# Performance work log

Hardware: AMD Instinct MI355X
Metric: run time of the kernel (lower is better)

Reference implementation:

```python
import jax, jax.numpy as jnp
import numpy as np

EPS = 1e-5
QMAX = 127.0   # 8-bit symmetric: representable range [-128, 127]
QMIN = -128.0


def ste_round(x):
    # straight-through rounding (identity gradient)
    return x + jax.lax.stop_gradient(jnp.round(x) - x)


def setup_inputs() -> dict:
    key = jax.random.key(0)
    ks = jax.random.split(key, 7)
    N, C_in, C_out, H, W = 64, 256, 128, 56, 56
    x = jax.random.normal(ks[0], (N, C_in, H, W), jnp.float32)
    act_scaling_factor = jax.random.uniform(ks[1], (1,), jnp.float32, 0.02, 0.08)
    bn_weight = 1.0 + 0.3 * jax.random.normal(ks[2], (C_in,), jnp.float32)
    bn_bias = 0.1 * jax.random.normal(ks[3], (C_in,), jnp.float32)
    bn_mean = 0.1 * jax.random.normal(ks[4], (C_in,), jnp.float32)
    bn_var = jax.random.uniform(ks[5], (C_in,), jnp.float32, 0.5, 1.5)
    conv_weight = 0.05 * jax.random.normal(ks[6], (C_out, C_in, 1, 1), jnp.float32)
    return {
        "x": x,
        "act_scaling_factor": act_scaling_factor,
        "bn_weight": bn_weight,
        "bn_bias": bn_bias,
        "bn_mean": bn_mean,
        "bn_var": bn_var,
        "conv_weight": conv_weight,
    }


def _fwd(x, act_scaling_factor, bn_weight, bn_bias, bn_mean, bn_var, conv_weight):
    act_sf = act_scaling_factor.reshape(())

    # ---- QuantBn: fold BN, quantize folded scale per-channel (8-bit symmetric) ----
    inv_std = jax.lax.rsqrt(bn_var + EPS)
    scale = bn_weight * inv_std                    # [C_in]
    shift = bn_bias - bn_mean * scale              # [C_in]
    bn_sf = jnp.max(jnp.abs(scale)) / QMAX         # per-tensor bn weight scale
    scale_q = jnp.clip(ste_round(scale / bn_sf), QMIN, QMAX) * bn_sf
    bias_sf = bn_sf * act_sf                        # bias quantized at combined scale
    shift_q = ste_round(shift / bias_sf) * bias_sf
    x = x * scale_q[None, :, None, None] + shift_q[None, :, None, None]

    # ---- ReLU ----
    x = jnp.maximum(x, 0.0)

    # ---- QuantAct 1: per-tensor symmetric 8-bit requant ----
    sf1 = jnp.max(jnp.abs(x)) / QMAX
    x = jnp.clip(ste_round(x / sf1), QMIN, QMAX) * sf1

    # ---- QuantConv2d: per-output-channel 8-bit symmetric weight quant, 1x1 conv ----
    w_sf = jnp.max(jnp.abs(conv_weight), axis=(1, 2, 3)) / QMAX   # [C_out]
    w_q = jnp.clip(ste_round(conv_weight / w_sf[:, None, None, None]), QMIN, QMAX) \
          * w_sf[:, None, None, None]
    y = jax.lax.conv_general_dilated(
        x, w_q, window_strides=(1, 1), padding='VALID',
        dimension_numbers=('NCHW', 'OIHW', 'NCHW'))

    # ---- QuantAct 2 ----
    sf2 = jnp.max(jnp.abs(y)) / QMAX
    y = jnp.clip(ste_round(y / sf2), QMIN, QMAX) * sf2

    # ---- QuantAveragePool2d (2x2, stride 2): average in integer domain, re-round ----
    N, C, H, W = y.shape
    y_int = (y / sf2).reshape(N, C, H // 2, 2, W // 2, 2).mean(axis=(3, 5))
    out = ste_round(y_int) * sf2
    return out, sf2


def reference(x, act_scaling_factor, bn_weight, bn_bias, bn_mean, bn_var, conv_weight):
    return _fwd(x, act_scaling_factor, bn_weight, bn_bias, bn_mean, bn_var, conv_weight)
```

## Files before the change

### kernel.cpp

```cpp
#include <hip/hip_runtime.h>

#define QMAXF 127.0f
typedef int i32x4 __attribute__((ext_vector_type(4)));

__device__ __forceinline__ unsigned fkey(float f) {
  const unsigned b = __float_as_uint(f);
  return (b & 0x80000000u) ? ~b : (b | 0x80000000u);
}
__device__ __forceinline__ float fdec(unsigned u) {
  return __uint_as_float((u & 0x80000000u) ? (u & 0x7FFFFFFFu) : ~u);
}

__global__ __launch_bounds__(256) void k0_zero(unsigned* __restrict__ p) {
  const int t = threadIdx.x;
  p[t] = 0u; p[t + 256] = 0u; p[t + 512] = 0u; p[t + 768] = 0u;
}

__global__ __launch_bounds__(256, 8) void k1_minmax(
    const float* __restrict__ x, const float* __restrict__ actsf,
    const float* __restrict__ bnw, const float* __restrict__ bnb,
    const float* __restrict__ bnm, const float* __restrict__ bnv,
    const float* __restrict__ cw, unsigned* __restrict__ chanKmx,
    unsigned* __restrict__ chanKmn, float* __restrict__ scq,
    float* __restrict__ shq, float* __restrict__ wsf,
    signed char* __restrict__ wq8) {
  const int t = threadIdx.x, b = blockIdx.x;
  if (b == 2048) {
    __shared__ float red[4];
    float scale, shift;
    {
#pragma clang fp contract(off)
      float inv = 1.0f / sqrtf(bnv[t] + 1e-5f);
      scale = bnw[t] * inv;
      float tmp = bnm[t] * scale;
      shift = bnb[t] - tmp;
    }
    float a = fabsf(scale);
    for (int o = 32; o > 0; o >>= 1) a = fmaxf(a, __shfl_xor(a, o));
    if ((t & 63) == 0) red[t >> 6] = a;
    __syncthreads();
    const float amax = fmaxf(fmaxf(red[0], red[1]), fmaxf(red[2], red[3]));
    const float bn_sf = amax / QMAXF;
    scq[t] = fminf(fmaxf(rintf(scale / bn_sf), -128.f), 127.f) * bn_sf;
    const float bias_sf = bn_sf * actsf[0];
    shq[t] = rintf(shift / bias_sf) * bias_sf;
    const int r = t >> 1, half = t & 1;
    const float4* wrow = (const float4*)(cw + r * 256 + half * 128);
    float mx = 0.f;
#pragma unroll
    for (int j = 0; j < 32; ++j) {
      const float4 v = wrow[j];
      mx = fmaxf(mx, fmaxf(fmaxf(fabsf(v.x), fabsf(v.y)), fmaxf(fabsf(v.z), fabsf(v.w))));
    }
    mx = fmaxf(mx, __shfl_xor(mx, 1));
    const float wsf_v = mx / QMAXF;
    if (half == 0) wsf[r] = wsf_v;
    int* w8w = (int*)wq8;
#pragma unroll
    for (int j = 0; j < 32; ++j) {
      const float4 v = wrow[j];
      const float q0 = fminf(fmaxf(rintf(v.x / wsf_v), -128.f), 127.f);
      const float q1 = fminf(fmaxf(rintf(v.y / wsf_v), -128.f), 127.f);
      const float q2 = fminf(fmaxf(rintf(v.z / wsf_v), -128.f), 127.f);
      const float q3 = fminf(fmaxf(rintf(v.w / wsf_v), -128.f), 127.f);
      w8w[r * 64 + half * 32 + j] =
          ((int)q0 & 255) | (((int)q1 & 255) << 8) | (((int)q2 & 255) << 16) | (((int)q3 & 255) << 24);
    }
    return;
  }
  __shared__ float redmn[4][8], redmx[4][8];
  const int n = b >> 5, cg = b & 31;
  const float4* __restrict__ x4 = (const float4*)x + (long)(n * 256 + cg * 8) * 784;
  float mn[8], mx[8];
#pragma unroll
  for (int r = 0; r < 8; ++r) { mn[r] = __builtin_inff(); mx[r] = -__builtin_inff(); }
#pragma unroll
  for (int r = 0; r < 8; ++r) {
    const float4* row = x4 + r * 784;
    for (int j = t; j < 784; j += 256) {
      const float4 v = row[j];
      mn[r] = fminf(mn[r], fminf(fminf(v.x, v.y), fminf(v.z, v.w)));
      mx[r] = fmaxf(mx[r], fmaxf(fmaxf(v.x, v.y), fmaxf(v.z, v.w)));
    }
  }
#pragma unroll
  for (int r = 0; r < 8; ++r)
    for (int o = 32; o > 0; o >>= 1) {
      mn[r] = fminf(mn[r], __shfl_xor(mn[r], o));
      mx[r] = fmaxf(mx[r], __shfl_xor(mx[r], o));
    }
  if ((t & 63) == 0) {
#pragma unroll
    for (int r = 0; r < 8; ++r) { redmn[t >> 6][r] = mn[r]; redmx[t >> 6][r] = mx[r]; }
  }
  __syncthreads();
  if (t < 8) {
    const float fmn = fminf(fminf(redmn[0][t], redmn[1][t]), fminf(redmn[2][t], redmn[3][t]));
    const float fmx = fmaxf(fmaxf(redmx[0][t], redmx[1][t]), fmaxf(redmx[2][t], redmx[3][t]));
    atomicMax(&chanKmx[cg * 8 + t], fkey(fmx));
    atomicMax(&chanKmn[cg * 8 + t], ~fkey(fmn));
  }
}

__global__ __launch_bounds__(256, 4) void k2f_quant_gemm(
    const float* __restrict__ x, const float* __restrict__ scq,
    const float* __restrict__ shq, const unsigned* __restrict__ chanKmx,
    const unsigned* __restrict__ chanKmn, const signed char* __restrict__ wq8,
    const float* __restrict__ wsf, signed char* __restrict__ xqT,
    float* __restrict__ blockmax) {
  __shared__ int sw[64 * 64];
  __shared__ float comax[128];
  __shared__ float red[4];
  __shared__ float sf1s;
  const int t = threadIdx.x, w = t >> 6, l = t & 63, m = l & 15, g = l >> 4;
  const int blk = blockIdx.x, n = blk / 49, tt = blk - n * 49;

  {
    const float s = scq[t], sh = shq[t];
    const float xe = (s >= 0.f) ? fdec(chanKmx[t]) : fdec(~chanKmn[t]);
    float z;
    {
#pragma clang fp contract(off)
      z = xe * s + sh;
    }
    float mm = fmaxf(z, 0.f);
    for (int o = 32; o > 0; o >>= 1) mm = fmaxf(mm, __shfl_xor(mm, o));
    if (l == 0) red[w] = mm;
    __syncthreads();
    if (t == 0) sf1s = fmaxf(fmaxf(red[0], red[1]), fmaxf(red[2], red[3])) / QMAXF;
    __syncthreads();
  }
  const float sf1 = sf1s;
  const float* __restrict__ xb = x + (long)n * 802816 + tt * 64;

  signed char* __restrict__ dst = xqT + ((long)(n * 3136 + tt * 64)) * 256;
  {
    const int slot = t & 15, hwq = t >> 4;
    const int hw0 = hwq * 4, ci0 = slot * 16;
    int wbuf[4][4] = {{0, 0, 0, 0}, {0, 0, 0, 0}, {0, 0, 0, 0}, {0, 0, 0, 0}};
#pragma unroll
    for (int j = 0; j < 16; ++j) {
      const float4 v = *(const float4*)(xb + (long)(ci0 + j) * 3136 + hw0);
      const float s = scq[ci0 + j], sh = shq[ci0 + j];
      float z0, z1, z2, z3;
      {
#pragma clang fp contract(off)
        z0 = v.x * s + sh; z1 = v.y * s + sh; z2 = v.z * s + sh; z3 = v.w * s + sh;
      }
      const float q0 = fminf(fmaxf(rintf(fmaxf(z0, 0.f) / sf1), -128.f), 127.f);
      const float q1 = fminf(fmaxf(rintf(fmaxf(z1, 0.f) / sf1), -128.f), 127.f);
      const float q2 = fminf(fmaxf(rintf(fmaxf(z2, 0.f) / sf1), -128.f), 127.f);
      const float q3 = fminf(fmaxf(rintf(fmaxf(z3, 0.f) / sf1), -128.f), 127.f);
      wbuf[0][j >> 2] |= ((int)q0 & 255) << ((j & 3) * 8);
      wbuf[1][j >> 2] |= ((int)q1 & 255) << ((j & 3) * 8);
      wbuf[2][j >> 2] |= ((int)q2 & 255) << ((j & 3) * 8);
      wbuf[3][j >> 2] |= ((int)q3 & 255) << ((j & 3) * 8);
    }
#pragma unroll
    for (int dh = 0; dh < 4; ++dh) {
      const int hw = hw0 + dh;
      *(i32x4*)&sw[hw * 64 + ((slot ^ (hw & 7)) << 2)] = *(const i32x4*)wbuf[dh];
      *(i32x4*)(dst + hw * 256 + slot * 16) = *(const i32x4*)wbuf[dh];
    }
  }
  __syncthreads();

  i32x4 acc[2][4];
#pragma unroll
  for (int ct = 0; ct < 2; ++ct)
#pragma unroll
    for (int ht = 0; ht < 4; ++ht) acc[ct][ht] = (i32x4){0, 0, 0, 0};
#pragma unroll
  for (int ks = 0; ks < 4; ++ks) {
    const i32x4 wf0 = *(const i32x4*)(wq8 + (w * 32 + m) * 256 + ks * 64 + g * 16);
    const i32x4 wf1 = *(const i32x4*)(wq8 + (w * 32 + 16 + m) * 256 + ks * 64 + g * 16);
#pragma unroll
    for (int ht = 0; ht < 4; ++ht) {
      const int row = ht * 16 + m;
      const i32x4 xf = *(const i32x4*)&sw[row * 64 + (((ks * 4 + g) ^ (row & 7)) << 2)];
      acc[0][ht] = __builtin_amdgcn_mfma_i32_16x16x64_i8(wf0, xf, acc[0][ht], 0, 0, 0);
      acc[1][ht] = __builtin_amdgcn_mfma_i32_16x16x64_i8(wf1, xf, acc[1][ht], 0, 0, 0);
    }
  }

  int im[2][4];
#pragma unroll
  for (int ct = 0; ct < 2; ++ct)
#pragma unroll
    for (int r = 0; r < 4; ++r) {
      int v = 0;
#pragma unroll
      for (int ht = 0; ht < 4; ++ht) {
        int a = acc[ct][ht][r];
        a = a < 0 ? -a : a;
        v = a > v ? a : v;
      }
      im[ct][r] = v;
    }
#pragma unroll
  for (int o = 1; o < 16; o <<= 1)
#pragma unroll
    for (int ct = 0; ct < 2; ++ct)
#pragma unroll
      for (int r = 0; r < 4; ++r) {
        const int other = __shfl_xor(im[ct][r], o);
        im[ct][r] = other > im[ct][r] ? other : im[ct][r];
      }
  if (m == 0) {
#pragma unroll
    for (int ct = 0; ct < 2; ++ct)
#pragma unroll
      for (int r = 0; r < 4; ++r)
        comax[w * 32 + ct * 16 + g * 4 + r] = (float)im[ct][r];
  }
  __syncthreads();
  float v = 0.f;
  if (t < 128) v = comax[t] * (sf1 * wsf[t]);
  for (int o = 32; o > 0; o >>= 1) v = fmaxf(v, __shfl_xor(v, o));
  if (l == 0) red[w] = v;
  __syncthreads();
  if (t == 0)
    blockmax[blk] = fmaxf(fmaxf(red[0], red[1]), fmaxf(red[2], red[3]));
}

__global__ __launch_bounds__(256, 3) void k3_final(
    const signed char* __restrict__ xqT, const signed char* __restrict__ wq8,
    const float* __restrict__ wsf, const float* __restrict__ scq,
    const float* __restrict__ shq, const unsigned* __restrict__ chanKmx,
    const unsigned* __restrict__ chanKmn, const float* __restrict__ blockmax,
    float* __restrict__ out, float* __restrict__ outsf2) {
  __shared__ _Float16 q2[128 * 116];
  __shared__ float red[4];
  __shared__ float sf1s, sf2s;
  const int t = threadIdx.x, w = t >> 6, l = t & 63;
  const int m = l & 15, g = l >> 4;
  const int blk = blockIdx.x;
  const int n = blk / 28, tt = blk - n * 28;

  {
    const float s = scq[t], sh = shq[t];
    const float xe = (s >= 0.f) ? fdec(chanKmx[t]) : fdec(~chanKmn[t]);
    float z;
    {
#pragma clang fp contract(off)
      z = xe * s + sh;
    }
    float mm = fmaxf(z, 0.f);
    for (int o = 32; o > 0; o >>= 1) mm = fmaxf(mm, __shfl_xor(mm, o));
    if (l == 0) red[w] = mm;
    __syncthreads();
    if (t == 0) sf1s = fmaxf(fmaxf(red[0], red[1]), fmaxf(red[2], red[3])) / QMAXF;
  }
  {
    float bm = 0.f;
    for (int i = t; i < 3136; i += 256) bm = fmaxf(bm, blockmax[i]);
    for (int o = 32; o > 0; o >>= 1) bm = fmaxf(bm, __shfl_xor(bm, o));
    __syncthreads();
    if (l == 0) red[w] = bm;
    __syncthreads();
    if (t == 0) sf2s = fmaxf(fmaxf(red[0], red[1]), fmaxf(red[2], red[3])) / QMAXF;
    __syncthreads();
  }
  const float sf1 = sf1s;
  const float sf2 = sf2s;
  if (blk == 0 && t == 0) outsf2[0] = sf2;

  const signed char* __restrict__ xb = xqT + ((long)(n * 3136 + tt * 112)) * 256;
  i32x4 acc[2][7];
#pragma unroll
  for (int ct = 0; ct < 2; ++ct)
#pragma unroll
    for (int ht = 0; ht < 7; ++ht) acc[ct][ht] = (i32x4){0, 0, 0, 0};
#pragma unroll
  for (int ks = 0; ks < 4; ++ks) {
    const i32x4 wf0 = *(const i32x4*)(wq8 + (w * 32 + m) * 256 + ks * 64 + g * 16);
    const i32x4 wf1 = *(const i32x4*)(wq8 + (w * 32 + 16 + m) * 256 + ks * 64 + g * 16);
#pragma unroll
    for (int ht = 0; ht < 7; ++ht) {
      const i32x4 xf = *(const i32x4*)(xb + (ht * 16 + m) * 256 + ks * 64 + g * 16);
      acc[0][ht] = __builtin_amdgcn_mfma_i32_16x16x64_i8(wf0, xf, acc[0][ht], 0, 0, 0);
      acc[1][ht] = __builtin_amdgcn_mfma_i32_16x16x64_i8(wf1, xf, acc[1][ht], 0, 0, 0);
    }
  }
  float fac[2][4];
#pragma unroll
  for (int ct = 0; ct < 2; ++ct)
#pragma unroll
    for (int r = 0; r < 4; ++r)
      fac[ct][r] = sf1 * wsf[w * 32 + ct * 16 + g * 4 + r];
#pragma unroll
  for (int ct = 0; ct < 2; ++ct)
#pragma unroll
    for (int ht = 0; ht < 7; ++ht)
#pragma unroll
      for (int r = 0; r < 4; ++r) {
        const float y = (float)acc[ct][ht][r] * fac[ct][r];
        const float q = fminf(fmaxf(rintf(y / sf2), -128.f), 127.f);
        q2[(w * 32 + ct * 16 + g * 4 + r) * 116 + ht * 16 + m] = (_Float16)q;
      }
  __syncthreads();
  const long obase = (long)n * 100352 + tt * 28;
  for (int i = t; i < 3584; i += 256) {
    const unsigned co = (unsigned)i / 28u;
    const unsigned wo = (unsigned)i - co * 28u;
    const _Float16* row = q2 + co * 116;
    const float a = (float)row[2 * wo] + (float)row[2 * wo + 1] +
                    (float)row[56 + 2 * wo] + (float)row[56 + 2 * wo + 1];
    out[obase + (long)co * 784 + wo] = rintf(a * 0.25f) * sf2;
  }
}

extern "C" void kernel_launch(void* const* d_in, const int* in_sizes, int n_in,
                              void* d_out, int out_size, void* d_ws, size_t ws_size,
                              hipStream_t stream) {
  const float* x     = (const float*)d_in[0];
  const float* actsf = (const float*)d_in[1];
  const float* bnw   = (const float*)d_in[2];
  const float* bnb   = (const float*)d_in[3];
  const float* bnm   = (const float*)d_in[4];
  const float* bnv   = (const float*)d_in[5];
  const float* cw    = (const float*)d_in[6];
  float* out = (float*)d_out;
  char* ws = (char*)d_ws;

  unsigned* chanKmx   = (unsigned*)(ws + 256);
  unsigned* chanKmn   = (unsigned*)(ws + 1280);
  float* scq          = (float*)(ws + 4096);
  float* shq          = (float*)(ws + 5120);
  float* wsf          = (float*)(ws + 6144);
  signed char* wq8    = (signed char*)(ws + 8192);
  float* blockmax     = (float*)(ws + 40960);
  signed char* xqT    = (signed char*)(ws + 65536);
  float* outsf2       = out + (out_size - 1);

  hipLaunchKernelGGL(k0_zero, dim3(1), dim3(256), 0, stream, (unsigned*)ws);
  hipLaunchKernelGGL(k1_minmax, dim3(2049), dim3(256), 0, stream,
                     x, actsf, bnw, bnb, bnm, bnv, cw, chanKmx, chanKmn, scq, shq, wsf, wq8);
  hipLaunchKernelGGL(k2f_quant_gemm, dim3(3136), dim3(256), 0, stream,
                     x, scq, shq, chanKmx, chanKmn, wq8, wsf, xqT, blockmax);
  hipLaunchKernelGGL(k3_final, dim3(1792), dim3(256), 0, stream,
                     xqT, wq8, wsf, scq, shq, chanKmx, chanKmn, blockmax, out, outsf2);
}
```

Baseline: 157.1 us.

## Enlarge quant-GEMM tile to 112 pixels with byte-granular swizzled LDS transpose

The fused quantize+GEMM kernel now processes 112 spatial positions per block instead of 64, cutting the grid from 3136 to 1792 blocks and the blockmax array accordingly. Loads are remapped so consecutive threads read contiguous float4 along HW, and quantized bytes are scattered into an XOR-swizzled LDS tile that is then read back as 16-byte rows both for the global xqT write and for the MFMA operands. BN scale/shift are cached in shared memory. The aim is better coalescing of x reads and fewer blocks, at the cost of byte-wide LDS stores, more LDS per block and more accumulator registers.

```diff
diff --git a/kernel.cpp b/kernel.cpp
--- a/kernel.cpp
+++ b/kernel.cpp
@@ -108,15 +108,17 @@
     const unsigned* __restrict__ chanKmn, const signed char* __restrict__ wq8,
     const float* __restrict__ wsf, signed char* __restrict__ xqT,
     float* __restrict__ blockmax) {
-  __shared__ int sw[64 * 64];
+  __shared__ __align__(16) unsigned char ldsb[112 * 256];
+  __shared__ float s_scq[256], s_shq[256];
   __shared__ float comax[128];
   __shared__ float red[4];
   __shared__ float sf1s;
   const int t = threadIdx.x, w = t >> 6, l = t & 63, m = l & 15, g = l >> 4;
-  const int blk = blockIdx.x, n = blk / 49, tt = blk - n * 49;
+  const int blk = blockIdx.x, n = blk / 28, tt = blk - n * 28;
 
   {
     const float s = scq[t], sh = shq[t];
+    s_scq[t] = s; s_shq[t] = sh;
     const float xe = (s >= 0.f) ? fdec(chanKmx[t]) : fdec(~chanKmn[t]);
     float z;
     {
@@ -131,53 +133,55 @@
     __syncthreads();
   }
   const float sf1 = sf1s;
-  const float* __restrict__ xb = x + (long)n * 802816 + tt * 64;
-
-  signed char* __restrict__ dst = xqT + ((long)(n * 3136 + tt * 64)) * 256;
-  {
-    const int slot = t & 15, hwq = t >> 4;
-    const int hw0 = hwq * 4, ci0 = slot * 16;
-    int wbuf[4][4] = {{0, 0, 0, 0}, {0, 0, 0, 0}, {0, 0, 0, 0}, {0, 0, 0, 0}};
-#pragma unroll
-    for (int j = 0; j < 16; ++j) {
-      const float4 v = *(const float4*)(xb + (long)(ci0 + j) * 3136 + hw0);
-      const float s = scq[ci0 + j], sh = shq[ci0 + j];
-      float z0, z1, z2, z3;
-      {
+  const float* __restrict__ xb = x + (long)n * 802816 + tt * 112;
+
+  for (int it = 0; it < 28; ++it) {
+    const int idx = it * 256 + t;
+    const int c = idx / 28;
+    const int p = idx - c * 28;
+    const float4 v = *(const float4*)(xb + (long)c * 3136 + 4 * p);
+    const float s = s_scq[c], sh = s_shq[c];
+    float z0, z1, z2, z3;
+    {
 #pragma clang fp contract(off)
-        z0 = v.x * s + sh; z1 = v.y * s + sh; z2 = v.z * s + sh; z3 = v.w * s + sh;
-      }
-      const float q0 = fminf(fmaxf(rintf(fmaxf(z0, 0.f) / sf1), -128.f), 127.f);
-      const float q1 = fminf(fmaxf(rintf(fmaxf(z1, 0.f) / sf1), -128.f), 127.f);
-      const float q2 = fminf(fmaxf(rintf(fmaxf(z2, 0.f) / sf1), -128.f), 127.f);
-      const float q3 = fminf(fmaxf(rintf(fmaxf(z3, 0.f) / sf1), -128.f), 127.f);
-      wbuf[0][j >> 2] |= ((int)q0 & 255) << ((j & 3) * 8);
-      wbuf[1][j >> 2] |= ((int)q1 & 255) << ((j & 3) * 8);
-      wbuf[2][j >> 2] |= ((int)q2 & 255) << ((j & 3) * 8);
-      wbuf[3][j >> 2] |= ((int)q3 & 255) << ((j & 3) * 8);
-    }
-#pragma unroll
-    for (int dh = 0; dh < 4; ++dh) {
-      const int hw = hw0 + dh;
-      *(i32x4*)&sw[hw * 64 + ((slot ^ (hw & 7)) << 2)] = *(const i32x4*)wbuf[dh];
-      *(i32x4*)(dst + hw * 256 + slot * 16) = *(const i32x4*)wbuf[dh];
-    }
-  }
-  __syncthreads();
-
-  i32x4 acc[2][4];
-#pragma unroll
-  for (int ct = 0; ct < 2; ++ct)
-#pragma unroll
-    for (int ht = 0; ht < 4; ++ht) acc[ct][ht] = (i32x4){0, 0, 0, 0};
+      z0 = v.x * s + sh; z1 = v.y * s + sh; z2 = v.z * s + sh; z3 = v.w * s + sh;
+    }
+    const float q0 = fminf(fmaxf(rintf(fmaxf(z0, 0.f) / sf1), -128.f), 127.f);
+    const float q1 = fminf(fmaxf(rintf(fmaxf(z1, 0.f) / sf1), -128.f), 127.f);
+    const float q2 = fminf(fmaxf(rintf(fmaxf(z2, 0.f) / sf1), -128.f), 127.f);
+    const float q3 = fminf(fmaxf(rintf(fmaxf(z3, 0.f) / sf1), -128.f), 127.f);
+    const int cs = c ^ ((p & 15) << 4);
+    const int hw0 = 4 * p;
+    ldsb[(hw0 + 0) * 256 + cs] = (unsigned char)((int)q0 & 255);
+    ldsb[(hw0 + 1) * 256 + cs] = (unsigned char)((int)q1 & 255);
+    ldsb[(hw0 + 2) * 256 + cs] = (unsigned char)((int)q2 & 255);
+    ldsb[(hw0 + 3) * 256 + cs] = (unsigned char)((int)q3 & 255);
+  }
+  __syncthreads();
+
+  signed char* __restrict__ dst = xqT + ((long)(n * 3136 + tt * 112)) * 256;
+#pragma unroll
+  for (int it = 0; it < 7; ++it) {
+    const int idx = it * 256 + t;
+    const int hw = idx >> 4, c16 = idx & 15;
+    const i32x4 v = *(const i32x4*)&ldsb[hw * 256 + ((c16 * 16) ^ (((hw >> 2) & 15) << 4))];
+    *(i32x4*)(dst + hw * 256 + c16 * 16) = v;
+  }
+
+  i32x4 acc[2][7];
+#pragma unroll
+  for (int ct = 0; ct < 2; ++ct)
+#pragma unroll
+    for (int ht = 0; ht < 7; ++ht) acc[ct][ht] = (i32x4){0, 0, 0, 0};
 #pragma unroll
   for (int ks = 0; ks < 4; ++ks) {
     const i32x4 wf0 = *(const i32x4*)(wq8 + (w * 32 + m) * 256 + ks * 64 + g * 16);
     const i32x4 wf1 = *(const i32x4*)(wq8 + (w * 32 + 16 + m) * 256 + ks * 64 + g * 16);
 #pragma unroll
-    for (int ht = 0; ht < 4; ++ht) {
+    for (int ht = 0; ht < 7; ++ht) {
       const int row = ht * 16 + m;
-      const i32x4 xf = *(const i32x4*)&sw[row * 64 + (((ks * 4 + g) ^ (row & 7)) << 2)];
+      const i32x4 xf = *(const i32x4*)&ldsb[row * 256 +
+                          ((ks * 64 + g * 16) ^ (((row >> 2) & 15) << 4))];
       acc[0][ht] = __builtin_amdgcn_mfma_i32_16x16x64_i8(wf0, xf, acc[0][ht], 0, 0, 0);
       acc[1][ht] = __builtin_amdgcn_mfma_i32_16x16x64_i8(wf1, xf, acc[1][ht], 0, 0, 0);
     }
@@ -190,7 +194,7 @@
     for (int r = 0; r < 4; ++r) {
       int v = 0;
 #pragma unroll
-      for (int ht = 0; ht < 4; ++ht) {
+      for (int ht = 0; ht < 7; ++ht) {
         int a = acc[ct][ht][r];
         a = a < 0 ? -a : a;
         v = a > v ? a : v;
@@ -253,7 +257,7 @@
   }
   {
     float bm = 0.f;
-    for (int i = t; i < 3136; i += 256) bm = fmaxf(bm, blockmax[i]);
+    for (int i = t; i < 1792; i += 256) bm = fmaxf(bm, blockmax[i]);
     for (int o = 32; o > 0; o >>= 1) bm = fmaxf(bm, __shfl_xor(bm, o));
     __syncthreads();
     if (l == 0) red[w] = bm;
@@ -336,7 +340,7 @@
   hipLaunchKernelGGL(k0_zero, dim3(1), dim3(256), 0, stream, (unsigned*)ws);
   hipLaunchKernelGGL(k1_minmax, dim3(2049), dim3(256), 0, stream,
                      x, actsf, bnw, bnb, bnm, bnv, cw, chanKmx, chanKmn, scq, shq, wsf, wq8);
-  hipLaunchKernelGGL(k2f_quant_gemm, dim3(3136), dim3(256), 0, stream,
+  hipLaunchKernelGGL(k2f_quant_gemm, dim3(1792), dim3(256), 0, stream,
                      x, scq, shq, chanKmx, chanKmn, wq8, wsf, xqT, blockmax);
   hipLaunchKernelGGL(k3_final, dim3(1792), dim3(256), 0, stream,
                      xqT, wq8, wsf, scq, shq, chanKmx, chanKmn, blockmax, out, outsf2);
```

Result: faster. 151.6 us (-3.5%).
